# Performance work log

Hardware: AMD Instinct MI355X
Metric: run time of the kernel (lower is better)

The kernel has to match this reference:

```python
import jax, jax.numpy as jnp
import numpy as np

N = 131072   # rows
D = 1024     # features per row
G = 16384    # number of index groups (all under label '0')
S = 8        # rows per group
PASS_COLS  = np.arange(0, 8)    # passthrough['0']: kept from original data
OTHER_COLS = np.arange(8, 16)   # passthrough['1']: label absent -> zero-filled


def setup_inputs() -> dict:
    key = jax.random.key(0)
    x = jax.random.normal(key, (N, D), dtype=jnp.float32)
    # Disjoint groups of S contiguous rows (sorted segment ids), covering all rows.
    segment_ids = jnp.repeat(jnp.arange(G, dtype=jnp.int64), S)
    return {"x": x, "segment_ids": segment_ids}


def reference(x, segment_ids):
    # Per-group mean (gather + mean-reduce), fully vectorized via segment_sum.
    sums = jax.ops.segment_sum(x, segment_ids, num_segments=G)            # [G, D]
    counts = jax.ops.segment_sum(jnp.ones((x.shape[0],), x.dtype),
                                 segment_ids, num_segments=G)             # [G]
    means = sums / counts[:, None]                                        # [G, D]
    out = means[segment_ids]                                              # broadcast mean back to rows
    # Selective column passthrough / zero-fill (scatter on columns as masks).
    pass_mask = jnp.zeros((D,), bool).at[jnp.asarray(PASS_COLS)].set(True)
    zero_mask = jnp.zeros((D,), bool).at[jnp.asarray(OTHER_COLS)].set(True)
    out = jnp.where(pass_mask[None, :], x, out)          # keep original data in passthrough cols
    out = jnp.where(zero_mask[None, :], jnp.zeros((), x.dtype), out)  # zero other_passthrough cols
    return out
```

## Files before the change

### kernel.cpp

```cpp
#include <hip/hip_runtime.h>


typedef float f32x4 __attribute__((ext_vector_type(4)));

__global__ __launch_bounds__(256) void selective_filter_kernel(
    const float* __restrict__ x, float* __restrict__ out) {
    const int g = blockIdx.x;
    const int t = threadIdx.x;
    const long long base = (long long)g * (8LL * 1024LL) + (long long)t * 4;

    const f32x4* __restrict__ xp = reinterpret_cast<const f32x4*>(x + base);
    f32x4* __restrict__ op = reinterpret_cast<f32x4*>(out + base);

    f32x4 v[8];
    f32x4 s = (f32x4)(0.f);
#pragma unroll
    for (int i = 0; i < 8; ++i) {
        v[i] = __builtin_nontemporal_load(xp + i * 256);
        s += v[i];
    }
    const f32x4 m = s * 0.125f;

    f32x4 o;
    if (t < 2) {
        o = (f32x4)(0.f);
    } else if (t < 4) {
        o = (f32x4)(0.f);
    } else {
        o = m;
    }

#pragma unroll
    for (int i = 0; i < 8; ++i) {
        f32x4 w = (t < 2) ? v[i] : o;
        __builtin_nontemporal_store(w, op + i * 256);
    }
}

extern "C" void kernel_launch(void* const* d_in, const int* in_sizes, int n_in,
                              void* d_out, int out_size, void* d_ws, size_t ws_size,
                              hipStream_t stream) {
    const float* x = (const float*)d_in[0];
    float* out = (float*)d_out;

    const int G = 16384;
    selective_filter_kernel<<<G, 256, 0, stream>>>(x, out);
}
```

Baseline: 193.8 us.

## Process eight groups per block with double-buffered register prefetch

Each block now handles eight consecutive groups instead of one, launching 2048 blocks rather than 16384. The kernel double-buffers the group rows in registers, issuing the next group's loads before reducing and storing the current one, so memory latency overlaps compute and stores. This cuts block launch overhead and keeps more loads in flight per thread. In exchange it doubles register use per thread and lowers the number of resident waves, which could reduce memory-level parallelism on this bandwidth-bound kernel.

```diff
diff --git a/kernel.cpp b/kernel.cpp
--- a/kernel.cpp
+++ b/kernel.cpp
@@ -3,37 +3,47 @@
 
 typedef float f32x4 __attribute__((ext_vector_type(4)));
 
+#define NBLK 2048
+#define GPB  8
+
 __global__ __launch_bounds__(256) void selective_filter_kernel(
     const float* __restrict__ x, float* __restrict__ out) {
-    const int g = blockIdx.x;
     const int t = threadIdx.x;
-    const long long base = (long long)g * (8LL * 1024LL) + (long long)t * 4;
+    const long long g0 = (long long)blockIdx.x * GPB;
+    const long long base0 = g0 * 8192LL + (long long)t * 4;
 
-    const f32x4* __restrict__ xp = reinterpret_cast<const f32x4*>(x + base);
-    f32x4* __restrict__ op = reinterpret_cast<f32x4*>(out + base);
+    const f32x4* __restrict__ xp = reinterpret_cast<const f32x4*>(x + base0);
+    f32x4* __restrict__ op = reinterpret_cast<f32x4*>(out + base0);
 
-    f32x4 v[8];
-    f32x4 s = (f32x4)(0.f);
-#pragma unroll
-    for (int i = 0; i < 8; ++i) {
-        v[i] = __builtin_nontemporal_load(xp + i * 256);
-        s += v[i];
-    }
-    const f32x4 m = s * 0.125f;
-
-    f32x4 o;
-    if (t < 2) {
-        o = (f32x4)(0.f);
-    } else if (t < 4) {
-        o = (f32x4)(0.f);
-    } else {
-        o = m;
-    }
+    f32x4 vA[8], vB[8];
 
 #pragma unroll
-    for (int i = 0; i < 8; ++i) {
-        f32x4 w = (t < 2) ? v[i] : o;
-        __builtin_nontemporal_store(w, op + i * 256);
+    for (int i = 0; i < 8; ++i)
+        vA[i] = __builtin_nontemporal_load(xp + i * 256);
+
+#pragma unroll
+    for (int k = 0; k < GPB; ++k) {
+        f32x4* v  = (k & 1) ? vB : vA;
+        f32x4* vn = (k & 1) ? vA : vB;
+
+        if (k < GPB - 1) {
+#pragma unroll
+            for (int i = 0; i < 8; ++i)
+                vn[i] = __builtin_nontemporal_load(xp + (k + 1) * 2048 + i * 256);
+        }
+
+        f32x4 s = (f32x4)(0.f);
+#pragma unroll
+        for (int i = 0; i < 8; ++i) s += v[i];
+        const f32x4 m = s * 0.125f;
+
+        const f32x4 zero = (f32x4)(0.f);
+        const f32x4 o = (t < 4) ? zero : m;
+#pragma unroll
+        for (int i = 0; i < 8; ++i) {
+            f32x4 w = (t < 2) ? v[i] : o;
+            __builtin_nontemporal_store(w, op + k * 2048 + i * 256);
+        }
     }
 }
 
@@ -43,6 +53,5 @@
     const float* x = (const float*)d_in[0];
     float* out = (float*)d_out;
 
-    const int G = 16384;
-    selective_filter_kernel<<<G, 256, 0, stream>>>(x, out);
+    selective_filter_kernel<<<NBLK, 256, 0, stream>>>(x, out);
 }
```

Result: no change. 194.0 us (+0.1%).
